# Performance work log

Measured on AMD Instinct MI355X. Metric: run time of the kernel, lower is better.

## Reference

```python
import jax, jax.numpy as jnp
import numpy as np
from jax import lax

B, N, K, NCP = 4, 2048, 20, 400
EPS = 1e-5


def _bn(x, gamma, beta, axes):
    # training-mode batch norm (biased variance), channel axis = 1
    m = jnp.mean(x, axis=axes, keepdims=True)
    v = jnp.var(x, axis=axes, keepdims=True)
    shape = [1] * x.ndim
    shape[1] = -1
    return (x - m) * lax.rsqrt(v + EPS) * gamma.reshape(shape) + beta.reshape(shape)


def _knn_idx(x, k):
    # x: [B, C, N] -> idx [B, N, k] (nearest, includes self like torch.cdist+topk(largest=False))
    x2 = jnp.sum(x * x, axis=1)  # [B, N]
    d = x2[:, :, None] + x2[:, None, :] - 2.0 * jnp.einsum('bcn,bcm->bnm', x, x)
    return lax.top_k(-d, k)[1]


def _edge_conv(x, w, gamma, beta, k):
    # x: [B, C, N], w: [O, 2C] -> [B, O, N] (1x1 conv + BN + LeakyReLU + max over k)
    idx = _knn_idx(x, k)                      # [B, N, k]
    xt = jnp.transpose(x, (0, 2, 1))          # [B, N, C]
    b = jnp.arange(xt.shape[0])[:, None, None]
    nbr = xt[b, idx]                          # [B, N, k, C]
    ctr = xt[:, :, None, :]
    feat = jnp.concatenate([nbr - ctr, jnp.broadcast_to(ctr, nbr.shape)], axis=-1)  # [B, N, k, 2C]
    y = jnp.einsum('bnkc,oc->bonk', feat, w)  # [B, O, N, k]
    y = jax.nn.leaky_relu(_bn(y, gamma, beta, axes=(0, 2, 3)), 0.2)
    return jnp.max(y, axis=-1)                # [B, O, N]


def setup_inputs() -> dict:
    key = jax.random.key(0)
    ks = jax.random.split(key, 16)
    rnd = lambda k_, s: jax.random.normal(k_, s, dtype=jnp.float32) * 0.02
    inp = {
        'x': jax.random.normal(ks[0], (B, 3, N), dtype=jnp.float32),
        'w1': rnd(ks[1], (64, 6)),    'g1': jnp.ones(64),   'b1': jnp.zeros(64),
        'w2': rnd(ks[2], (128, 128)), 'g2': jnp.ones(128),  'b2': jnp.zeros(128),
        'w3': rnd(ks[3], (256, 256)), 'g3': jnp.ones(256),  'b3': jnp.zeros(256),
        'w4': rnd(ks[4], (512, 512)), 'g4': jnp.ones(512),  'b4': jnp.zeros(512),
        'w5': rnd(ks[5], (2048, 963)), 'g5': jnp.ones(2048), 'b5': jnp.zeros(2048),
        'w6': rnd(ks[6], (2048, 2048)), 'wb6': jnp.zeros(2048), 'g6': jnp.ones(2048), 'b6': jnp.zeros(2048),
        'w7': rnd(ks[7], (4096, 4096)), 'wb7': jnp.zeros(4096), 'g7': jnp.ones(4096), 'b7': jnp.zeros(4096),
        'w8': rnd(ks[8], (NCP, 4096)), 'wb8': jnp.zeros(NCP),
    }
    return inp


def reference(x, w1, g1, b1, w2, g2, b2, w3, g3, b3, w4, g4, b4,
              w5, g5, b5, w6, wb6, g6, b6, w7, wb7, g7, b7, w8, wb8):
    x0 = x                                            # [B, 3, N]
    x1 = _edge_conv(x0, w1, g1, b1, K)                # [B, 64, N]
    x2 = _edge_conv(x1, w2, g2, b2, K)                # [B, 128, N]
    x3 = _edge_conv(x2, w3, g3, b3, K)                # [B, 256, N]
    x4 = _edge_conv(x3, w4, g4, b4, K)                # [B, 512, N]
    h = jnp.concatenate([x0, x1, x2, x3, x4], axis=1) # [B, 963, N]
    h = jnp.einsum('bcn,oc->bon', h, w5)              # [B, 2048, N]
    h = jax.nn.leaky_relu(_bn(h, g5, b5, axes=(0, 2)), 0.2)
    p = jnp.max(h, axis=-1, keepdims=True)            # [B, 2048, 1] global max pool
    y = jnp.einsum('bcl,oc->bol', p, w6) + wb6[None, :, None]
    y = jax.nn.relu(_bn(y, g6, b6, axes=(0, 2)))
    y = jnp.concatenate([y, p], axis=1)               # [B, 4096, 1]
    y = jnp.einsum('bcl,oc->bol', y, w7) + wb7[None, :, None]
    y = jax.nn.relu(_bn(y, g7, b7, axes=(0, 2)))
    y = jnp.einsum('bcl,oc->bol', y, w8) + wb8[None, :, None]
    return jnp.tanh(y[:, :, 0])                       # [B, NCP]
```

## Files before the change

kernel.cpp:

```cpp
#include <hip/hip_runtime.h>
#include <float.h>
#include <math.h>


#define NPTS 2048
#define BATCH 4
#define KNN 20
#define CH_H 963
#define KPAD 992
#define HSTRIDE (CH_H*NPTS)

typedef _Float16 half8 __attribute__((ext_vector_type(8)));
typedef float f32x4 __attribute__((ext_vector_type(4)));

typedef const __attribute__((address_space(1))) unsigned int* gas_p;
typedef __attribute__((address_space(3))) unsigned int* las_p;
__device__ __forceinline__ void gl_lds16(const void* g, void* l){
  __builtin_amdgcn_global_load_lds((gas_p)g, (las_p)l, 16, 0, 0);
}

__device__ __forceinline__ unsigned fenc(float x){
  unsigned u = __float_as_uint(x);
  return (u & 0x80000000u) ? ~u : (u | 0x80000000u);
}
__device__ __forceinline__ float fdec(unsigned u){
  u = (u & 0x80000000u) ? (u ^ 0x80000000u) : ~u;
  return __uint_as_float(u);
}

__global__ void k_convert(const float* __restrict__ x, float* __restrict__ H){
  int i = blockIdx.x*256 + threadIdx.x;
  if (i >= BATCH*3*NPTS) return;
  int b = i / (3*NPTS); int r = i % (3*NPTS);
  H[(size_t)b*HSTRIDE + r] = x[i];
}

__global__ void k_norms(const float* __restrict__ X, int C, float* __restrict__ X2,
                        float* __restrict__ SUMZ){
  int i = blockIdx.x*256 + threadIdx.x;
  if (i < 1024) SUMZ[i] = 0.f;
  int b = i >> 11, n = i & 2047;
  const float* Xb = X + (size_t)b*HSTRIDE + n;
  float s = 0.f;
  for (int c=0;c<C;++c){ float v = Xb[(size_t)c*NPTS]; s = fmaf(v,v,s); }
  X2[i] = s;
}

__global__ __launch_bounds__(256) void k_xsplit(const float* __restrict__ X, int C, int Cpad,
        _Float16* __restrict__ Xhi, _Float16* __restrict__ Xlo)
{
  __shared__ float t[64][65];
  int b = blockIdx.z;
  int n0 = blockIdx.x*64, c0 = blockIdx.y*64;
  int tid = threadIdx.x; int l = tid & 63, m = tid >> 6;
  for (int cc = m; cc < 64; cc += 4){
    int c = c0 + cc;
    t[cc][l] = (c < C) ? X[(size_t)b*HSTRIDE + (size_t)c*NPTS + n0 + l] : 0.f;
  }
  __syncthreads();
  for (int nn = m; nn < 64; nn += 4){
    int c = c0 + l;
    if (c < Cpad){
      float v = t[l][nn];
      _Float16 h = (_Float16)v;
      size_t o = ((size_t)(b<<11)+n0+nn)*Cpad + c;
      Xhi[o] = h;
      Xlo[o] = (_Float16)(v - (float)h);
    }
  }
}

__global__ __launch_bounds__(256) void k_gram(const _Float16* __restrict__ Xhi,
        const _Float16* __restrict__ Xlo, int Cpad, int bbase,
        float* __restrict__ G0, float* __restrict__ G1)
{
  __shared__ half8 AsH[2][128][4]; __shared__ half8 AsL[2][128][4];
  __shared__ half8 BsH[2][128][4]; __shared__ half8 BsL[2][128][4];
  int bl = blockIdx.z;
  int b  = bbase + bl;
  float* G = bl ? G1 : G0;
  const _Float16* Hb = Xhi + (size_t)(b<<11)*Cpad;
  const _Float16* Lb = Xlo + (size_t)(b<<11)*Cpad;
  int m0 = blockIdx.x*128, n0 = blockIdx.y*128;
  int tid = threadIdx.x;
  int w = tid>>6, lane = tid&63;
  int wm = w>>1, wn = w&1;
  int quad = lane>>4, col = lane&15;
  int wbase = w*128;
  f32x4 acc[4][4];
  #pragma unroll
  for (int i=0;i<4;++i)
    #pragma unroll
    for (int j=0;j<4;++j) acc[i][j] = (f32x4){0.f,0.f,0.f,0.f};

  auto stageg = [&](int buf, int k0){
    #pragma unroll
    for (int i=0;i<2;++i){
      int cid = wbase + i*64 + lane;
      int row = cid>>2, kc = cid&3;
      size_t ao = (size_t)(n0+row)*Cpad + k0 + kc*8;
      size_t bo = (size_t)(m0+row)*Cpad + k0 + kc*8;
      int lo = (wbase + i*64)*16;
      gl_lds16(Hb + ao, (char*)&AsH[buf][0][0] + lo);
      gl_lds16(Lb + ao, (char*)&AsL[buf][0][0] + lo);
      gl_lds16(Hb + bo, (char*)&BsH[buf][0][0] + lo);
      gl_lds16(Lb + bo, (char*)&BsL[buf][0][0] + lo);
    }
  };

  int NT = Cpad >> 5;
  stageg(0, 0);
  if (NT > 1) stageg(1, 32);
  for (int kt=0; kt<NT; ++kt){
    int buf = kt & 1;
    if (kt+1 < NT) asm volatile("s_waitcnt vmcnt(8)" ::: "memory");
    else           asm volatile("s_waitcnt vmcnt(0)" ::: "memory");
    __builtin_amdgcn_s_barrier();
    __builtin_amdgcn_sched_barrier(0);
    half8 ah[4], al[4], bh[4], blo[4];
    #pragma unroll
    for (int mt=0;mt<4;++mt){ ah[mt] = AsH[buf][wm*64 + mt*16 + col][quad];
                              al[mt] = AsL[buf][wm*64 + mt*16 + col][quad]; }
    #pragma unroll
    for (int nt=0;nt<4;++nt){ bh[nt] = BsH[buf][wn*64 + nt*16 + col][quad];
                              blo[nt] = BsL[buf][wn*64 + nt*16 + col][quad]; }
    #pragma unroll
    for (int mt=0;mt<4;++mt)
      #pragma unroll
      for (int nt=0;nt<4;++nt){
        acc[mt][nt] = __builtin_amdgcn_mfma_f32_16x16x32_f16(ah[mt], bh[nt], acc[mt][nt], 0, 0, 0);
        acc[mt][nt] = __builtin_amdgcn_mfma_f32_16x16x32_f16(ah[mt], blo[nt], acc[mt][nt], 0, 0, 0);
        acc[mt][nt] = __builtin_amdgcn_mfma_f32_16x16x32_f16(al[mt], bh[nt], acc[mt][nt], 0, 0, 0);
      }
    __builtin_amdgcn_sched_barrier(0);
    __builtin_amdgcn_s_barrier();
    if (kt+2 < NT) stageg(buf, (kt+2)<<5);
  }
  #pragma unroll
  for (int mt=0;mt<4;++mt){
    #pragma unroll
    for (int r=0;r<4;++r){
      int n = n0 + wm*64 + mt*16 + quad*4 + r;
      #pragma unroll
      for (int nt=0;nt<4;++nt){
        int m = m0 + wn*64 + nt*16 + col;
        G[(size_t)n*2048 + m] = acc[mt][nt][r];
      }
    }
  }
}

#define KNN_CH(OPC) OPC(0) OPC(1) OPC(2) OPC(3) OPC(4) OPC(5) OPC(6) OPC(7)
#define DECL_CH(ch) float d##ch##_0,d##ch##_1,d##ch##_2,d##ch##_3;
#define LOADG_CH(ch) { float4 g = *(const float4*)(grow + (ch)*256 + base); \
  float4 xm = *(const float4*)(x2b + (ch)*256 + base); \
  d##ch##_0 = x2n + xm.x - 2.f*g.x; d##ch##_1 = x2n + xm.y - 2.f*g.y; \
  d##ch##_2 = x2n + xm.z - 2.f*g.z; d##ch##_3 = x2n + xm.w - 2.f*g.w; }
#define DECL_G(ch) float gv##ch; int gm##ch;
#define MKCH(ch) { gv##ch = d##ch##_0; gm##ch = (ch)*256 + base; \
  if (d##ch##_1 < gv##ch){ gv##ch = d##ch##_1; gm##ch = (ch)*256 + base + 1; } \
  if (d##ch##_2 < gv##ch){ gv##ch = d##ch##_2; gm##ch = (ch)*256 + base + 2; } \
  if (d##ch##_3 < gv##ch){ gv##ch = d##ch##_3; gm##ch = (ch)*256 + base + 3; } }
#define REMCASE(ch) case ch: { \
  if (own){ if (cp==0) d##ch##_0 = FLT_MAX; else if (cp==1) d##ch##_1 = FLT_MAX; \
            else if (cp==2) d##ch##_2 = FLT_MAX; else d##ch##_3 = FLT_MAX; } \
  MKCH(ch) } break;

__global__ __launch_bounds__(256,4) void k_sel(const float* __restrict__ G0,
        const float* __restrict__ G1, const float* __restrict__ X2,
        int bbase, int* __restrict__ IDX)
{
  int tid = threadIdx.x;
  int w = tid >> 6, lane = tid & 63;
  int n = blockIdx.x*4 + w;
  int b = bbase + blockIdx.y;
  const float* grow = (blockIdx.y ? G1 : G0) + (size_t)n*2048;
  const float* x2b  = X2 + (b<<11);
  float x2n = x2b[n];
  int base = lane << 2;
  KNN_CH(DECL_CH)
  KNN_CH(LOADG_CH)
  KNN_CH(DECL_G)
  KNN_CH(MKCH)
  int* op = IDX + ((size_t)(b<<11)+n)*KNN;
  for (int it=0; it<KNN; ++it){
    float v = fminf(fminf(fminf(gv0,gv1),fminf(gv2,gv3)),
                    fminf(fminf(gv4,gv5),fminf(gv6,gv7)));
    #pragma unroll
    for (int s=1; s<64; s<<=1) v = fminf(v, __shfl_xor(v, s));
    int mc = 0x7fffffff;
    mc = (gv7==v) ? gm7 : mc;
    mc = (gv6==v) ? gm6 : mc;
    mc = (gv5==v) ? gm5 : mc;
    mc = (gv4==v) ? gm4 : mc;
    mc = (gv3==v) ? gm3 : mc;
    mc = (gv2==v) ? gm2 : mc;
    mc = (gv1==v) ? gm1 : mc;
    mc = (gv0==v) ? gm0 : mc;
    int m = mc;
    #pragma unroll
    for (int s=1; s<64; s<<=1) m = min(m, __shfl_xor(m, s));
    if (lane==0) op[it] = m;
    int sm = __builtin_amdgcn_readfirstlane(m);
    bool own = (lane == ((sm>>2)&63));
    int cp = sm & 3;
    switch (sm >> 8){ KNN_CH(REMCASE) }
  }
}

__global__ __launch_bounds__(256) void k_vu(const float* __restrict__ X,
        const float* __restrict__ W, int C, int O,
        float* __restrict__ V, float* __restrict__ U)
{
  __shared__ float Xs[8][128];
  __shared__ float Wdv[8][64];
  __shared__ float Wuv[8][64];
  int b = blockIdx.z, n0 = blockIdx.x*128, o0 = blockIdx.y*64;
  int tid = threadIdx.x;
  int tj = tid & 15, ti = tid >> 4;
  float4 aV[8], aU[8];
  #pragma unroll
  for (int i=0;i<8;++i){ aV[i]=make_float4(0,0,0,0); aU[i]=make_float4(0,0,0,0); }
  const float* Xb = X + (size_t)b*HSTRIDE;
  for (int c0=0;c0<C;c0+=8){
    {
      int cc = tid >> 5, nn = (tid & 31) * 4; int c = c0 + cc;
      float4 v = (c<C) ? *(const float4*)(Xb + (size_t)c*NPTS + n0 + nn)
                       : make_float4(0,0,0,0);
      *(float4*)&Xs[cc][nn] = v;
    }
    for (int l=tid;l<512;l+=256){
      int oo=l>>3, cc=l&7, c=c0+cc;
      float wd=0.f, wu=0.f;
      if (c<C){
        const float* wr = W + (size_t)(o0+oo)*(2*C);
        wd = wr[c]; wu = wr[C+c] - wd;
      }
      Wdv[cc][oo]=wd; Wuv[cc][oo]=wu;
    }
    __syncthreads();
    #pragma unroll
    for (int cc=0;cc<8;++cc){
      float4 x0 = *(float4*)&Xs[cc][ti*8];
      float4 x1 = *(float4*)&Xs[cc][ti*8+4];
      float4 wd = *(float4*)&Wdv[cc][tj*4];
      float4 wu = *(float4*)&Wuv[cc][tj*4];
      float xs[8] = {x0.x,x0.y,x0.z,x0.w,x1.x,x1.y,x1.z,x1.w};
      #pragma unroll
      for (int i=0;i<8;++i){
        aV[i].x = fmaf(xs[i], wd.x, aV[i].x);
        aV[i].y = fmaf(xs[i], wd.y, aV[i].y);
        aV[i].z = fmaf(xs[i], wd.z, aV[i].z);
        aV[i].w = fmaf(xs[i], wd.w, aV[i].w);
        aU[i].x = fmaf(xs[i], wu.x, aU[i].x);
        aU[i].y = fmaf(xs[i], wu.y, aU[i].y);
        aU[i].z = fmaf(xs[i], wu.z, aU[i].z);
        aU[i].w = fmaf(xs[i], wu.w, aU[i].w);
      }
    }
    __syncthreads();
  }
  #pragma unroll
  for (int i=0;i<8;++i){
    int n = n0 + ti*8 + i;
    size_t basep = ((size_t)b*NPTS + n)*O + o0 + tj*4;
    *(float4*)(V+basep) = aV[i];
    *(float4*)(U+basep) = aU[i];
  }
}

template<int OC, int CHN>
__global__ __launch_bounds__(256) void k_gather(const float* __restrict__ V,
        const float* __restrict__ U, const int* __restrict__ IDX,
        float* __restrict__ YMX, float* __restrict__ YMN,
        float* __restrict__ SUM, float* __restrict__ SUMSQ)
{
  constexpr int O = OC*CHN;
  constexpr int NT = 8;
  constexpr int NSTEP = 256/OC;
  __shared__ int sidx[NT*KNN];
  __shared__ float rs[256], rq[256];
  int bid = blockIdx.x;
  int xcd  = bid & 7;
  int b    = xcd >> 1;
  int half = xcd & 1;
  int r    = bid >> 3;
  int ngrp, chunk;
  if (CHN == 1){ ngrp = (half<<7) | r; chunk = 0; }
  else         { ngrp = r & 255; chunk = half*(CHN/2) + (r>>8); }
  int n0 = ngrp * NT;
  int tid = threadIdx.x;
  for (int l = tid; l < NT*KNN; l += 256)
    sidx[l] = IDX[((size_t)(b<<11)+n0)*KNN + l];
  __syncthreads();
  int o  = chunk*OC + (tid & (OC-1));
  int ns = tid / OC;
  const float* Vb = V + (size_t)(b<<11)*O + o;
  float s = 0.f, q = 0.f;
  #pragma unroll
  for (int i = 0; i < NT/NSTEP; ++i){
    int nn = ns + i*NSTEP;
    int n = n0 + nn;
    size_t ub = ((size_t)(b<<11)+n)*O + o;
    float sv = 0.f, sv2 = 0.f, mx = -FLT_MAX, mn = FLT_MAX;
    #pragma unroll
    for (int k=0;k<KNN;++k){
      int m = sidx[nn*KNN+k];
      float v = Vb[(size_t)m*O];
      mx = fmaxf(mx,v); mn = fminf(mn,v);
      sv += v; sv2 = fmaf(v,v,sv2);
    }
    float u = __builtin_nontemporal_load(U + ub);
    __builtin_nontemporal_store(mx + u, YMX + ub);
    __builtin_nontemporal_store(mn + u, YMN + ub);
    s += sv + (float)KNN * u;
    q += sv2 + 2.f*u*sv + (float)KNN*u*u;
  }
  rs[tid] = s; rq[tid] = q;
  __syncthreads();
  if (tid < OC){
    #pragma unroll
    for (int t=1; t<NSTEP; ++t){ s += rs[tid + t*OC]; q += rq[tid + t*OC]; }
    atomicAdd(&SUM[o], s);
    atomicAdd(&SUMSQ[o], q);
  }
}

__global__ void k_finalize(const float* __restrict__ SUM, const float* __restrict__ SUMSQ,
        const float* __restrict__ g, const float* __restrict__ bt,
        int O, float invM, float* __restrict__ SC, float* __restrict__ SH){
  int o = blockIdx.x*256 + threadIdx.x;
  if (o>=O) return;
  float m = SUM[o]*invM;
  float var = SUMSQ[o]*invM - m*m;
  float sc = g[o] * rsqrtf(var + 1e-5f);
  SC[o]=sc; SH[o] = bt[o] - m*sc;
}

__global__ __launch_bounds__(256) void k_apply(const float* __restrict__ YMX, const float* __restrict__ YMN,
        const float* __restrict__ SC, const float* __restrict__ SH,
        int O, float* __restrict__ OUT)
{
  __shared__ float t[64][65];
  int b = blockIdx.z;
  int o0 = blockIdx.y*64, n0 = blockIdx.x*64;
  int tid = threadIdx.x;
  int lo = tid & 63, ln = tid >> 6;
  float sc = SC[o0+lo], sh = SH[o0+lo];
  for (int nn = ln; nn < 64; nn += 4){
    size_t idx = ((size_t)(b<<11)+n0+nn)*O + o0 + lo;
    float v = (sc >= 0.f) ? YMX[idx] : YMN[idx];
    float y = fmaf(sc, v, sh);
    y = (y > 0.f) ? y : 0.2f*y;
    t[lo][nn] = y;
  }
  __syncthreads();
  for (int oo = ln; oo < 64; oo += 4){
    OUT[(size_t)b*HSTRIDE + (size_t)(o0+oo)*NPTS + n0 + lo] = t[oo][lo];
  }
}

__global__ __launch_bounds__(256) void k_h2f16(const float* __restrict__ H, _Float16* __restrict__ Hf){
  __shared__ float t[64][65];
  int b = blockIdx.z;
  int n0 = blockIdx.x*64, c0 = blockIdx.y*64;
  int tid = threadIdx.x; int l = tid & 63, m = tid >> 6;
  for (int cc = m; cc < 64; cc += 4){
    int c = c0 + cc;
    t[cc][l] = (c < CH_H) ? H[(size_t)b*HSTRIDE + (size_t)c*NPTS + n0 + l] : 0.f;
  }
  __syncthreads();
  for (int nn = m; nn < 64; nn += 4){
    int c = c0 + l;
    if (c < KPAD)
      Hf[((size_t)(b<<11)+n0+nn)*KPAD + c] = (_Float16)t[l][nn];
  }
}

__global__ void k_w5f16(const float* __restrict__ w5, _Float16* __restrict__ Wf,
                        unsigned* __restrict__ z){
  int i = blockIdx.x*256 + threadIdx.x;
  if (i < 12288) z[i] = 0u;
  else if (i < 20480) z[i] = 0xFFFFFFFFu;
  if (i >= 2048*KPAD) return;
  int o = i / KPAD, c = i - o*KPAD;
  Wf[i] = (c < CH_H) ? (_Float16)w5[(size_t)o*CH_H + c] : (_Float16)0.f;
}

__global__ __launch_bounds__(256) void k_l5mfma(const _Float16* __restrict__ Wf,
        const _Float16* __restrict__ Hf,
        float* __restrict__ SUM5, float* __restrict__ SUMSQ5,
        unsigned* __restrict__ MAXB, unsigned* __restrict__ MINB)
{
  __shared__ half8 As[2][128][4];
  __shared__ half8 Bs[2][128][4];
  int b  = blockIdx.z;
  int n0 = blockIdx.x*128, o0 = blockIdx.y*128;
  int tid = threadIdx.x;
  int w = tid>>6, lane = tid&63;
  int wm = w>>1, wn = w&1;
  int quad = lane>>4, col = lane&15;
  int wbase = w*128;
  f32x4 acc[4][4];
  #pragma unroll
  for (int i=0;i<4;++i)
    #pragma unroll
    for (int j=0;j<4;++j) acc[i][j] = (f32x4){0.f,0.f,0.f,0.f};

  auto stage5 = [&](int buf, int k0){
    #pragma unroll
    for (int i=0;i<2;++i){
      int cid = wbase + i*64 + lane;
      int row = cid>>2, kc = cid&3;
      int lo = (wbase + i*64)*16;
      gl_lds16(Wf + (size_t)(o0+row)*KPAD + k0 + kc*8, (char*)&As[buf][0][0] + lo);
      gl_lds16(Hf + ((size_t)(b<<11)+n0+row)*KPAD + k0 + kc*8, (char*)&Bs[buf][0][0] + lo);
    }
  };

  const int NT = KPAD/32;
  stage5(0, 0);
  stage5(1, 32);
  for (int kt=0; kt<NT; ++kt){
    int buf = kt & 1;
    if (kt+1 < NT) asm volatile("s_waitcnt vmcnt(4)" ::: "memory");
    else           asm volatile("s_waitcnt vmcnt(0)" ::: "memory");
    __builtin_amdgcn_s_barrier();
    __builtin_amdgcn_sched_barrier(0);
    half8 af[4], bf[4];
    #pragma unroll
    for (int mt=0;mt<4;++mt) af[mt] = As[buf][wm*64 + mt*16 + col][quad];
    #pragma unroll
    for (int nt=0;nt<4;++nt) bf[nt] = Bs[buf][wn*64 + nt*16 + col][quad];
    #pragma unroll
    for (int mt=0;mt<4;++mt)
      #pragma unroll
      for (int nt=0;nt<4;++nt)
        acc[mt][nt] = __builtin_amdgcn_mfma_f32_16x16x32_f16(af[mt], bf[nt], acc[mt][nt], 0, 0, 0);
    __builtin_amdgcn_sched_barrier(0);
    __builtin_amdgcn_s_barrier();
    if (kt+2 < NT) stage5(buf, (kt+2)*32);
  }
  #pragma unroll
  for (int mt=0;mt<4;++mt){
    #pragma unroll
    for (int r=0;r<4;++r){
      float s=0.f, q=0.f, mx=-FLT_MAX, mn=FLT_MAX;
      #pragma unroll
      for (int nt=0;nt<4;++nt){
        float y = acc[mt][nt][r];
        s += y; q = fmaf(y,y,q);
        mx = fmaxf(mx,y); mn = fminf(mn,y);
      }
      #pragma unroll
      for (int d=8; d; d>>=1){
        s += __shfl_down(s,(unsigned)d,16);
        q += __shfl_down(q,(unsigned)d,16);
        mx = fmaxf(mx,__shfl_down(mx,(unsigned)d,16));
        mn = fminf(mn,__shfl_down(mn,(unsigned)d,16));
      }
      if (col==0){
        int o = o0 + wm*64 + mt*16 + quad*4 + r;
        atomicAdd(&SUM5[o], s);
        atomicAdd(&SUMSQ5[o], q);
        atomicMax(&MAXB[(b<<11)+o], fenc(mx));
        atomicMin(&MINB[(b<<11)+o], fenc(mn));
      }
    }
  }
}

__global__ void k_l5_final(const float* __restrict__ SUM5, const float* __restrict__ SUMSQ5,
        const unsigned* __restrict__ MAXB, const unsigned* __restrict__ MINB,
        const float* __restrict__ g5, const float* __restrict__ b5, float* __restrict__ P)
{
  int o = blockIdx.x*256 + threadIdx.x;
  if (o>=2048) return;
  float m = SUM5[o]*(1.f/8192.f);
  float var = SUMSQ5[o]*(1.f/8192.f) - m*m;
  float sc = g5[o] * rsqrtf(var + 1e-5f);
  float sh = b5[o] - m*sc;
  for (int b=0;b<4;++b){
    float mx = fdec(MAXB[b*2048+o]);
    float mn = fdec(MINB[b*2048+o]);
    float v = (sc >= 0.f) ? fmaf(sc,mx,sh) : fmaf(sc,mn,sh);
    v = (v > 0.f) ? v : 0.2f*v;
    P[b*2048 + o] = v;
  }
}

__global__ __launch_bounds__(256) void k_fc(const float* __restrict__ W, const float* __restrict__ bias,
        const float* __restrict__ Z, int Cin, int O, float* __restrict__ Y)
{
  int o = blockIdx.x*4 + (threadIdx.x>>6);
  int lane = threadIdx.x & 63;
  if (o >= O) return;
  const float* wr = W + (size_t)o*Cin;
  float a0=0.f,a1=0.f,a2=0.f,a3=0.f;
  for (int c=lane;c<Cin;c+=64){
    float w = wr[c];
    a0 = fmaf(w, Z[c],        a0);
    a1 = fmaf(w, Z[Cin+c],    a1);
    a2 = fmaf(w, Z[2*Cin+c],  a2);
    a3 = fmaf(w, Z[3*Cin+c],  a3);
  }
  #pragma unroll
  for (int s=32;s;s>>=1){
    a0 += __shfl_down(a0,(unsigned)s); a1 += __shfl_down(a1,(unsigned)s);
    a2 += __shfl_down(a2,(unsigned)s); a3 += __shfl_down(a3,(unsigned)s);
  }
  if (lane==0){
    float bb = bias[o];
    Y[o]=a0+bb; Y[O+o]=a1+bb; Y[2*O+o]=a2+bb; Y[3*O+o]=a3+bb;
  }
}

__global__ void k_bn4(const float* __restrict__ Y, const float* __restrict__ g, const float* __restrict__ bt,
                      int O, float* __restrict__ Z, int zstride, int zoff)
{
  int o = blockIdx.x*256 + threadIdx.x;
  if (o>=O) return;
  float v0=Y[o], v1=Y[O+o], v2=Y[2*O+o], v3=Y[3*O+o];
  float m = 0.25f*(v0+v1+v2+v3);
  float d0=v0-m, d1=v1-m, d2=v2-m, d3=v3-m;
  float var = 0.25f*(d0*d0+d1*d1+d2*d2+d3*d3);
  float sc = g[o] * rsqrtf(var + 1e-5f);
  float sh = bt[o] - m*sc;
  Z[0*zstride+zoff+o] = fmaxf(fmaf(sc,v0,sh), 0.f);
  Z[1*zstride+zoff+o] = fmaxf(fmaf(sc,v1,sh), 0.f);
  Z[2*zstride+zoff+o] = fmaxf(fmaf(sc,v2,sh), 0.f);
  Z[3*zstride+zoff+o] = fmaxf(fmaf(sc,v3,sh), 0.f);
}

__global__ void k_copy_p(const float* __restrict__ P, float* __restrict__ Z){
  int i = blockIdx.x*256 + threadIdx.x;
  int b = i>>11, o = i&2047;
  Z[b*4096 + 2048 + o] = P[i];
}

__global__ __launch_bounds__(256) void k_final(const float* __restrict__ W8, const float* __restrict__ wb8,
        const float* __restrict__ Z7, float* __restrict__ out)
{
  int o = blockIdx.x*4 + (threadIdx.x>>6);
  int lane = threadIdx.x & 63;
  if (o >= 400) return;
  const float* wr = W8 + (size_t)o*4096;
  float a0=0.f,a1=0.f,a2=0.f,a3=0.f;
  for (int c=lane;c<4096;c+=64){
    float w = wr[c];
    a0 = fmaf(w, Z7[c],        a0);
    a1 = fmaf(w, Z7[4096+c],   a1);
    a2 = fmaf(w, Z7[2*4096+c], a2);
    a3 = fmaf(w, Z7[3*4096+c], a3);
  }
  #pragma unroll
  for (int s=32;s;s>>=1){
    a0 += __shfl_down(a0,(unsigned)s); a1 += __shfl_down(a1,(unsigned)s);
    a2 += __shfl_down(a2,(unsigned)s); a3 += __shfl_down(a3,(unsigned)s);
  }
  if (lane==0){
    float bb = wb8[o];
    out[0*400+o] = tanhf(a0+bb);
    out[1*400+o] = tanhf(a1+bb);
    out[2*400+o] = tanhf(a2+bb);
    out[3*400+o] = tanhf(a3+bb);
  }
}

extern "C" void kernel_launch(void* const* d_in, const int* in_sizes, int n_in,
                              void* d_out, int out_size, void* d_ws, size_t ws_size,
                              hipStream_t stream)
{
  const float* x   = (const float*)d_in[0];
  const float* w_e[4]  = {(const float*)d_in[1], (const float*)d_in[4], (const float*)d_in[7], (const float*)d_in[10]};
  const float* g_e[4]  = {(const float*)d_in[2], (const float*)d_in[5], (const float*)d_in[8], (const float*)d_in[11]};
  const float* b_e[4]  = {(const float*)d_in[3], (const float*)d_in[6], (const float*)d_in[9], (const float*)d_in[12]};
  const float* w5  = (const float*)d_in[13];
  const float* g5  = (const float*)d_in[14];
  const float* b5  = (const float*)d_in[15];
  const float* w6  = (const float*)d_in[16];
  const float* wb6 = (const float*)d_in[17];
  const float* g6  = (const float*)d_in[18];
  const float* b6  = (const float*)d_in[19];
  const float* w7  = (const float*)d_in[20];
  const float* wb7 = (const float*)d_in[21];
  const float* g7  = (const float*)d_in[22];
  const float* b7  = (const float*)d_in[23];
  const float* w8  = (const float*)d_in[24];
  const float* wb8 = (const float*)d_in[25];

  float* WS = (float*)d_ws;
  float* H    = WS;
  float* V    = WS + 7888896;
  float* U    = V  + 4194304;
  float* YMX  = U  + 4194304;
  float* YMN  = YMX+ 4194304;
  int*   IDX  = (int*)(YMN + 4194304);
  float* X2   = (float*)(IDX + 163840);
  float* SUM  = X2 + 8192;
  float* SUMSQ= SUM + 512;
  float* SC   = SUMSQ + 512;
  float* SH   = SC + 512;
  float* SUM5 = SH + 512;
  float* SUMSQ5 = SUM5 + 2048;
  unsigned* MAXB = (unsigned*)(SUMSQ5 + 2048);
  unsigned* MINB = MAXB + 8192;
  float* P    = (float*)(MINB + 8192);
  float* Y6   = P + 8192;
  float* Z    = Y6 + 8192;
  float* Y7   = Z + 16384;
  float* Z7   = Y7 + 16384;
  _Float16* Hf  = (_Float16*)V;
  _Float16* Wf  = (_Float16*)U;
  _Float16* Xhi = (_Float16*)U;
  _Float16* Xlo = (_Float16*)U + 4*2048*256;
  float* G0 = YMX;
  float* G1 = YMN;

  k_convert<<<96,256,0,stream>>>(x, H);

  const int Cin_[4]  = {3,64,128,256};
  const int Cpad_[4] = {32,64,128,256};
  const int O_[4]    = {64,128,256,512};
  const int ioff_[4] = {0,3,67,195};
  const int ooff_[4] = {3,67,195,451};

  for (int l=0;l<4;++l){
    const float* Xl = H + (size_t)ioff_[l]*NPTS;
    int C = Cin_[l], Cpad = Cpad_[l], O = O_[l];
    k_norms<<<32,256,0,stream>>>(Xl, C, X2, SUM);
    dim3 gxs(32, (Cpad+63)/64, 4);
    k_xsplit<<<gxs,256,0,stream>>>(Xl, C, Cpad, Xhi, Xlo);
    dim3 ggr(16,16,2);
    k_gram<<<ggr,256,0,stream>>>(Xhi, Xlo, Cpad, 0, G0, G1);
    dim3 gsl(512,2);
    k_sel<<<gsl,256,0,stream>>>(G0, G1, X2, 0, IDX);
    k_gram<<<ggr,256,0,stream>>>(Xhi, Xlo, Cpad, 2, G0, G1);
    k_sel<<<gsl,256,0,stream>>>(G0, G1, X2, 2, IDX);
    dim3 gvu(16, O/64, 4);
    k_vu<<<gvu,256,0,stream>>>(Xl, w_e[l], C, O, V, U);
    if (O == 64)
      k_gather<64,1><<<1024,256,0,stream>>>(V, U, IDX, YMX, YMN, SUM, SUMSQ);
    else if (O == 128)
      k_gather<128,1><<<1024,256,0,stream>>>(V, U, IDX, YMX, YMN, SUM, SUMSQ);
    else if (O == 256)
      k_gather<128,2><<<2048,256,0,stream>>>(V, U, IDX, YMX, YMN, SUM, SUMSQ);
    else
      k_gather<128,4><<<4096,256,0,stream>>>(V, U, IDX, YMX, YMN, SUM, SUMSQ);
    k_finalize<<<2,256,0,stream>>>(SUM, SUMSQ, g_e[l], b_e[l], O, 1.f/163840.f, SC, SH);
    dim3 gap(32, O/64, 4);
    k_apply<<<gap,256,0,stream>>>(YMX, YMN, SC, SH, O, H + (size_t)ooff_[l]*NPTS);
  }

  dim3 gtr(32,16,4);
  k_h2f16<<<gtr,256,0,stream>>>(H, Hf);
  k_w5f16<<<(2048*KPAD+255)/256,256,0,stream>>>(w5, Wf, (unsigned*)SUM5);
  dim3 g5g(16,16,4);
  k_l5mfma<<<g5g,256,0,stream>>>(Wf, Hf, SUM5, SUMSQ5, MAXB, MINB);
  k_l5_final<<<8,256,0,stream>>>(SUM5, SUMSQ5, MAXB, MINB, g5, b5, P);

  k_fc<<<512,256,0,stream>>>(w6, wb6, P, 2048, 2048, Y6);
  k_bn4<<<8,256,0,stream>>>(Y6, g6, b6, 2048, Z, 4096, 0);
  k_copy_p<<<32,256,0,stream>>>(P, Z);
  k_fc<<<1024,256,0,stream>>>(w7, wb7, Z, 4096, 4096, Y7);
  k_bn4<<<16,256,0,stream>>>(Y7, g7, b7, 4096, Z7, 4096, 0);
  k_final<<<100,256,0,stream>>>(w8, wb8, Z7, (float*)d_out);
}
```

Baseline: 1.065 ms.

## Compute edge-conv V/U projections with split-fp16 MFMA instead of scalar FP32

Replaces the scalar FP32 FMA kernel for the per-point V/U projections with an MFMA kernel. It reuses the hi/lo fp16 split of X already produced for the Gram step and adds a new kernel that splits the weights into [Wd; Wu-Wd] hi/lo halves. Three MFMAs per tile approximate FP32 accuracy, and scratch buffers are reassigned so the split X survives until the projection. This adds a small weight-split launch per layer and gives a slightly different rounding behaviour than plain FP32.

New measurement: 1.001 ms. 6.0% less time.

```diff
diff --git a/kernel.cpp b/kernel.cpp
--- a/kernel.cpp
+++ b/kernel.cpp
@@ -68,6 +68,20 @@
       Xlo[o] = (_Float16)(v - (float)h);
     }
   }
+}
+
+__global__ void k_wsplit(const float* __restrict__ W, int C, int Cpad, int O,
+        _Float16* __restrict__ Wh, _Float16* __restrict__ Wl){
+  int i = blockIdx.x*256 + threadIdx.x;
+  if (i >= 2*O*Cpad) return;
+  int op = i / Cpad, c = i - op*Cpad;
+  float v = 0.f;
+  if (c < C){
+    const float* wr = W + (size_t)(op < O ? op : op - O)*(2*C);
+    v = (op < O) ? wr[c] : (wr[C+c] - wr[c]);
+  }
+  _Float16 h = (_Float16)v;
+  Wh[i] = h; Wl[i] = (_Float16)(v - (float)h);
 }
 
 __global__ __launch_bounds__(256) void k_gram(const _Float16* __restrict__ Xhi,
@@ -145,6 +159,88 @@
       for (int nt=0;nt<4;++nt){
         int m = m0 + wn*64 + nt*16 + col;
         G[(size_t)n*2048 + m] = acc[mt][nt][r];
+      }
+    }
+  }
+}
+
+__global__ __launch_bounds__(256) void k_vu_mfma(const _Float16* __restrict__ Xh,
+        const _Float16* __restrict__ Xl, const _Float16* __restrict__ Wh,
+        const _Float16* __restrict__ Wl, int Cpad, int O,
+        float* __restrict__ V, float* __restrict__ U)
+{
+  __shared__ half8 AsH[2][128][4]; __shared__ half8 AsL[2][128][4];
+  __shared__ half8 BsH[2][128][4]; __shared__ half8 BsL[2][128][4];
+  int b = blockIdx.z;
+  const _Float16* Hb = Xh + (size_t)(b<<11)*Cpad;
+  const _Float16* Lb = Xl + (size_t)(b<<11)*Cpad;
+  int n0 = blockIdx.x*128, o0 = blockIdx.y*128;
+  int tid = threadIdx.x;
+  int w = tid>>6, lane = tid&63;
+  int wm = w>>1, wn = w&1;
+  int quad = lane>>4, col = lane&15;
+  int wbase = w*128;
+  f32x4 acc[4][4];
+  #pragma unroll
+  for (int i=0;i<4;++i)
+    #pragma unroll
+    for (int j=0;j<4;++j) acc[i][j] = (f32x4){0.f,0.f,0.f,0.f};
+
+  auto stagev = [&](int buf, int k0){
+    #pragma unroll
+    for (int i=0;i<2;++i){
+      int cid = wbase + i*64 + lane;
+      int row = cid>>2, kc = cid&3;
+      size_t ao = (size_t)(n0+row)*Cpad + k0 + kc*8;
+      size_t bo = (size_t)(o0+row)*Cpad + k0 + kc*8;
+      int lo = (wbase + i*64)*16;
+      gl_lds16(Hb + ao, (char*)&AsH[buf][0][0] + lo);
+      gl_lds16(Lb + ao, (char*)&AsL[buf][0][0] + lo);
+      gl_lds16(Wh + bo, (char*)&BsH[buf][0][0] + lo);
+      gl_lds16(Wl + bo, (char*)&BsL[buf][0][0] + lo);
+    }
+  };
+
+  int NT = Cpad >> 5;
+  stagev(0, 0);
+  if (NT > 1) stagev(1, 32);
+  for (int kt=0; kt<NT; ++kt){
+    int buf = kt & 1;
+    if (kt+1 < NT) asm volatile("s_waitcnt vmcnt(8)" ::: "memory");
+    else           asm volatile("s_waitcnt vmcnt(0)" ::: "memory");
+    __builtin_amdgcn_s_barrier();
+    __builtin_amdgcn_sched_barrier(0);
+    half8 ah[4], al[4], bh[4], blo[4];
+    #pragma unroll
+    for (int mt=0;mt<4;++mt){ ah[mt] = AsH[buf][wm*64 + mt*16 + col][quad];
+                              al[mt] = AsL[buf][wm*64 + mt*16 + col][quad]; }
+    #pragma unroll
+    for (int nt=0;nt<4;++nt){ bh[nt] = BsH[buf][wn*64 + nt*16 + col][quad];
+                              blo[nt] = BsL[buf][wn*64 + nt*16 + col][quad]; }
+    #pragma unroll
+    for (int mt=0;mt<4;++mt)
+      #pragma unroll
+      for (int nt=0;nt<4;++nt){
+        acc[mt][nt] = __builtin_amdgcn_mfma_f32_16x16x32_f16(ah[mt], bh[nt], acc[mt][nt], 0, 0, 0);
+        acc[mt][nt] = __builtin_amdgcn_mfma_f32_16x16x32_f16(ah[mt], blo[nt], acc[mt][nt], 0, 0, 0);
+        acc[mt][nt] = __builtin_amdgcn_mfma_f32_16x16x32_f16(al[mt], bh[nt], acc[mt][nt], 0, 0, 0);
+      }
+    __builtin_amdgcn_sched_barrier(0);
+    __builtin_amdgcn_s_barrier();
+    if (kt+2 < NT) stagev(buf, (kt+2)<<5);
+  }
+  #pragma unroll
+  for (int mt=0;mt<4;++mt){
+    #pragma unroll
+    for (int r=0;r<4;++r){
+      int n = n0 + wm*64 + mt*16 + quad*4 + r;
+      size_t R = (size_t)(b<<11) + n;
+      #pragma unroll
+      for (int nt=0;nt<4;++nt){
+        int op = o0 + wn*64 + nt*16 + col;
+        float y = acc[mt][nt][r];
+        if (op < O) V[R*O + op] = y;
+        else        U[R*O + op - O] = y;
       }
     }
   }
@@ -205,67 +301,6 @@
     bool own = (lane == ((sm>>2)&63));
     int cp = sm & 3;
     switch (sm >> 8){ KNN_CH(REMCASE) }
-  }
-}
-
-__global__ __launch_bounds__(256) void k_vu(const float* __restrict__ X,
-        const float* __restrict__ W, int C, int O,
-        float* __restrict__ V, float* __restrict__ U)
-{
-  __shared__ float Xs[8][128];
-  __shared__ float Wdv[8][64];
-  __shared__ float Wuv[8][64];
-  int b = blockIdx.z, n0 = blockIdx.x*128, o0 = blockIdx.y*64;
-  int tid = threadIdx.x;
-  int tj = tid & 15, ti = tid >> 4;
-  float4 aV[8], aU[8];
-  #pragma unroll
-  for (int i=0;i<8;++i){ aV[i]=make_float4(0,0,0,0); aU[i]=make_float4(0,0,0,0); }
-  const float* Xb = X + (size_t)b*HSTRIDE;
-  for (int c0=0;c0<C;c0+=8){
-    {
-      int cc = tid >> 5, nn = (tid & 31) * 4; int c = c0 + cc;
-      float4 v = (c<C) ? *(const float4*)(Xb + (size_t)c*NPTS + n0 + nn)
-                       : make_float4(0,0,0,0);
-      *(float4*)&Xs[cc][nn] = v;
-    }
-    for (int l=tid;l<512;l+=256){
-      int oo=l>>3, cc=l&7, c=c0+cc;
-      float wd=0.f, wu=0.f;
-      if (c<C){
-        const float* wr = W + (size_t)(o0+oo)*(2*C);
-        wd = wr[c]; wu = wr[C+c] - wd;
-      }
-      Wdv[cc][oo]=wd; Wuv[cc][oo]=wu;
-    }
-    __syncthreads();
-    #pragma unroll
-    for (int cc=0;cc<8;++cc){
-      float4 x0 = *(float4*)&Xs[cc][ti*8];
-      float4 x1 = *(float4*)&Xs[cc][ti*8+4];
-      float4 wd = *(float4*)&Wdv[cc][tj*4];
-      float4 wu = *(float4*)&Wuv[cc][tj*4];
-      float xs[8] = {x0.x,x0.y,x0.z,x0.w,x1.x,x1.y,x1.z,x1.w};
-      #pragma unroll
-      for (int i=0;i<8;++i){
-        aV[i].x = fmaf(xs[i], wd.x, aV[i].x);
-        aV[i].y = fmaf(xs[i], wd.y, aV[i].y);
-        aV[i].z = fmaf(xs[i], wd.z, aV[i].z);
-        aV[i].w = fmaf(xs[i], wd.w, aV[i].w);
-        aU[i].x = fmaf(xs[i], wu.x, aU[i].x);
-        aU[i].y = fmaf(xs[i], wu.y, aU[i].y);
-        aU[i].z = fmaf(xs[i], wu.z, aU[i].z);
-        aU[i].w = fmaf(xs[i], wu.w, aU[i].w);
-      }
-    }
-    __syncthreads();
-  }
-  #pragma unroll
-  for (int i=0;i<8;++i){
-    int n = n0 + ti*8 + i;
-    size_t basep = ((size_t)b*NPTS + n)*O + o0 + tj*4;
-    *(float4*)(V+basep) = aV[i];
-    *(float4*)(U+basep) = aU[i];
   }
 }
 
@@ -612,10 +647,12 @@
   float* Z7   = Y7 + 16384;
   _Float16* Hf  = (_Float16*)V;
   _Float16* Wf  = (_Float16*)U;
-  _Float16* Xhi = (_Float16*)U;
-  _Float16* Xlo = (_Float16*)U + 4*2048*256;
+  _Float16* Xhi  = (_Float16*)YMN;
+  _Float16* Xlo  = Xhi + (size_t)4*2048*256;
+  _Float16* Wsph = Xlo + (size_t)4*2048*256;
+  _Float16* Wspl = Wsph + 1024*256;
   float* G0 = YMX;
-  float* G1 = YMN;
+  float* G1 = V;
 
   k_convert<<<96,256,0,stream>>>(x, H);
 
@@ -631,14 +668,15 @@
     k_norms<<<32,256,0,stream>>>(Xl, C, X2, SUM);
     dim3 gxs(32, (Cpad+63)/64, 4);
     k_xsplit<<<gxs,256,0,stream>>>(Xl, C, Cpad, Xhi, Xlo);
+    k_wsplit<<<(2*O*Cpad+255)/256,256,0,stream>>>(w_e[l], C, Cpad, O, Wsph, Wspl);
     dim3 ggr(16,16,2);
     k_gram<<<ggr,256,0,stream>>>(Xhi, Xlo, Cpad, 0, G0, G1);
     dim3 gsl(512,2);
     k_sel<<<gsl,256,0,stream>>>(G0, G1, X2, 0, IDX);
     k_gram<<<ggr,256,0,stream>>>(Xhi, Xlo, Cpad, 2, G0, G1);
     k_sel<<<gsl,256,0,stream>>>(G0, G1, X2, 2, IDX);
-    dim3 gvu(16, O/64, 4);
-    k_vu<<<gvu,256,0,stream>>>(Xl, w_e[l], C, O, V, U);
+    dim3 gvm(16, (2*O)/128, 4);
+    k_vu_mfma<<<gvm,256,0,stream>>>(Xhi, Xlo, Wsph, Wspl, Cpad, O, V, U);
     if (O == 64)
       k_gather<64,1><<<1024,256,0,stream>>>(V, U, IDX, YMX, YMN, SUM, SUMSQ);
     else if (O == 128)
```
